# Performance work log

Measured on AMD Instinct MI355X. Metric: run time of the kernel, lower is better.

Reference implementation:

```python
import jax, jax.numpy as jnp
import numpy as np

# dims
B, L, H, W, C = 1, 5, 100, 176, 256   # batch, agents, BEV height, BEV width, channels
HEADS, DHEAD, T = 8, 32, 3            # heads, per-head dim, num agent types
D = HEADS * DHEAD                     # == C here (to_qkv inner dim)
SCALE = DHEAD ** -0.5


def setup_inputs() -> dict:
    key = jax.random.key(0)
    ks = jax.random.split(key, 14)
    x = jax.random.normal(ks[0], (B, L, H, W, C), jnp.float32)
    mask = jnp.ones((B, H, W, 1, L), jnp.int32)
    types = jax.random.randint(ks[1], (B, L), 0, T)
    # prior_encoding: [B, L, 1, 1, 3] = (velocity, dt, type); only type (channel 2) is used
    prior_encoding = jnp.zeros((B, L, 1, 1, 3), jnp.float32).at[..., 2].set(
        types[:, :, None, None].astype(jnp.float32))
    s = C ** -0.5
    Wq = jax.random.normal(ks[2], (T, C, D), jnp.float32) * s
    bq = jax.random.normal(ks[3], (T, D), jnp.float32) * 0.01
    Wk = jax.random.normal(ks[4], (T, C, D), jnp.float32) * s
    bk = jax.random.normal(ks[5], (T, D), jnp.float32) * 0.01
    Wv = jax.random.normal(ks[6], (T, C, D), jnp.float32) * s
    bv = jax.random.normal(ks[7], (T, D), jnp.float32) * 0.01
    Wa = jax.random.normal(ks[8], (T, D, C), jnp.float32) * (D ** -0.5)
    ba = jax.random.normal(ks[9], (T, C), jnp.float32) * 0.01
    rel_att = jax.random.normal(ks[10], (T * T, HEADS, DHEAD, DHEAD), jnp.float32) * (DHEAD ** -0.5)
    rel_msg = jax.random.normal(ks[11], (T * T, HEADS, DHEAD, DHEAD), jnp.float32) * (DHEAD ** -0.5)
    return dict(x=x, mask=mask, prior_encoding=prior_encoding,
                Wq=Wq, bq=bq, Wk=Wk, bk=bk, Wv=Wv, bv=bv, Wa=Wa, ba=ba,
                rel_att=rel_att, rel_msg=rel_msg)


def _split_heads(t):
    # [B,H,W,L,D] -> [B,m,H,W,L,p]
    return jnp.transpose(t.reshape(B, H, W, L, HEADS, DHEAD), (0, 4, 1, 2, 3, 5))


def reference(x, mask, prior_encoding, Wq, bq, Wk, bk, Wv, bv, Wa, ba, rel_att, rel_msg):
    types = prior_encoding[:, :, 0, 0, 2].astype(jnp.int32)      # [B,L]
    xp = jnp.transpose(x, (0, 2, 3, 1, 4))                        # [B,H,W,L,C]

    def proj(Wt, bt):
        # per-agent-type linear: gather weights per agent, then batched matmul
        return jnp.einsum('bhwlc,blcd->bhwld', xp, Wt[types]) + bt[types][:, None, None]

    q = _split_heads(proj(Wq, bq))                                # [B,m,H,W,L,p]
    k = _split_heads(proj(Wk, bk))
    v = _split_heads(proj(Wv, bv))

    etype = types[:, :, None] * T + types[:, None, :]             # [B,L,L]
    w_att = jnp.transpose(rel_att[etype], (0, 3, 1, 2, 4, 5))     # [B,m,L,L,p,q]
    w_msg = jnp.transpose(rel_msg[etype], (0, 3, 1, 2, 4, 5))     # [B,m,L,L,p,c]

    att = jnp.einsum('bmhwip,bmijpq,bmhwjq->bmhwij', q, w_att, k) * SCALE
    att = jnp.where(mask[:, None] == 0, -jnp.inf, att)            # mask [B,1,H,W,1,L]
    att = jax.nn.softmax(att, axis=-1)

    v_msg = jnp.einsum('bmijpc,bmhwjp->bmhwijc', w_msg, v)        # relation-weighted messages
    out = jnp.einsum('bmhwij,bmhwijc->bmhwic', att, v_msg)        # [B,m,H,W,L,c]

    out = jnp.transpose(out, (0, 2, 3, 4, 1, 5)).reshape(B, H, W, L, D)
    out = jnp.einsum('bhwld,bldc->bhwlc', out, Wa[types]) + ba[types][:, None, None]
    return jnp.transpose(out, (0, 3, 1, 2, 4))                    # [B,L,H,W,C]
```

## Files before the change

### kernel.cpp

```cpp
#include <hip/hip_runtime.h>
#include <math.h>

#define HW     17600
#define CD     256
#define LAG    5
#define NHEAD  8
#define DH     32
#define NT     3

typedef short bf16x8 __attribute__((ext_vector_type(8)));
typedef float f32x4  __attribute__((ext_vector_type(4)));

__device__ __forceinline__ float bflo(unsigned u) { return __uint_as_float(u << 16); }
__device__ __forceinline__ float bfhi(unsigned u) { return __uint_as_float(u & 0xffff0000u); }
__device__ __forceinline__ unsigned f2bf(float f) {
    unsigned u = __float_as_uint(f);
    return (u + 0x7fffu + ((u >> 16) & 1u)) >> 16;
}
__device__ __forceinline__ unsigned pack2(float a, float b) {
    return f2bf(a) | (f2bf(b) << 16);
}

__global__ __launch_bounds__(256) void convert_w_kernel(
    const float* __restrict__ Wq, const float* __restrict__ Wk,
    const float* __restrict__ Wv, const float* __restrict__ Wa,
    unsigned short* __restrict__ Wt)
{
    __shared__ float tile[64][65];
    const int mat = blockIdx.y;
    const int k0 = (blockIdx.x >> 2) * 64;
    const int n0 = (blockIdx.x & 3) * 64;
    const float* W;
    if      (mat < 3) W = Wq + (long)mat * 65536;
    else if (mat < 6) W = Wk + (long)(mat - 3) * 65536;
    else if (mat < 9) W = Wv + (long)(mat - 6) * 65536;
    else              W = Wa + (long)(mat - 9) * 65536;
    const int t = threadIdx.x;
#pragma unroll
    for (int r = 0; r < 16; ++r) {
        int idx = r * 256 + t;
        int row = idx >> 6, col = idx & 63;
        tile[row][col] = W[(long)(k0 + row) * 256 + n0 + col];
    }
    __syncthreads();
    unsigned short* dst = Wt + (long)mat * 65536;
#pragma unroll
    for (int r = 0; r < 16; ++r) {
        int idx = r * 256 + t;
        int row = idx >> 6, col = idx & 63;
        dst[(long)(n0 + row) * 256 + k0 + col] = (unsigned short)f2bf(tile[col][row]);
    }
}

__global__ __launch_bounds__(256) void convert_rel_kernel(
    const float* __restrict__ rel_att, const float* __restrict__ rel_msg,
    unsigned short* __restrict__ rattT, unsigned short* __restrict__ rmsgT)
{
    const long base = ((long)(blockIdx.x * NHEAD + blockIdx.y)) << 10;
    const int t = threadIdx.x;
#pragma unroll
    for (int i = 0; i < 4; ++i) {
        int idx = t * 4 + i;
        int p = idx >> 5, q = idx & 31;
        rattT[base + q * 32 + p] = (unsigned short)f2bf(rel_att[base + idx]);
        rmsgT[base + q * 32 + p] = (unsigned short)f2bf(rel_msg[base + idx]);
    }
}

template<bool AF32, bool YBF>
__device__ __forceinline__ void gemm_mfma_core(
    const void* __restrict__ Aptr, long lda,
    const unsigned short* __restrict__ Wt,
    const float* __restrict__ bias,
    void* __restrict__ Yptr, long ldy)
{
    __shared__ unsigned short As[64 * 64];
    __shared__ unsigned short Ws[256 * 64];

    const int t  = threadIdx.x;
    const int m0 = blockIdx.x * 64;
    const int w  = t >> 6;
    const int l  = t & 63;
    const int wr = w >> 1;
    const int wc = w & 1;
    const int fr = l & 15;
    const int ko = (l >> 4) << 3;

    const int srow = t >> 3;
    const int colu = (t & 7) << 3;
    const int scol = colu ^ ((srow & 7) << 3);
    const int axor = (fr & 7) << 3;

    f32x4 acc[2][8];
#pragma unroll
    for (int i = 0; i < 2; ++i)
#pragma unroll
        for (int j = 0; j < 8; ++j) {
            acc[i][j][0] = 0.f; acc[i][j][1] = 0.f;
            acc[i][j][2] = 0.f; acc[i][j][3] = 0.f;
        }

    for (int ks = 0; ks < 4; ++ks) {
        const int k0 = ks << 6;
        __syncthreads();
#pragma unroll
        for (int r = 0; r < 2; ++r) {
            int row = r * 32 + srow;
            if (AF32) {
                const float* src = (const float*)Aptr + (long)(m0 + row) * lda + k0 + colu;
                float4 f0 = *(const float4*)src;
                float4 f1 = *(const float4*)(src + 4);
                uint4 u;
                u.x = pack2(f0.x, f0.y); u.y = pack2(f0.z, f0.w);
                u.z = pack2(f1.x, f1.y); u.w = pack2(f1.z, f1.w);
                *(uint4*)(&As[row * 64 + scol]) = u;
            } else {
                const unsigned short* src =
                    (const unsigned short*)Aptr + (long)(m0 + row) * lda + k0 + colu;
                *(uint4*)(&As[row * 64 + scol]) = *(const uint4*)src;
            }
        }
#pragma unroll
        for (int r = 0; r < 8; ++r) {
            int row = r * 32 + srow;
            *(uint4*)(&Ws[row * 64 + scol]) =
                *(const uint4*)(Wt + (long)row * 256 + k0 + colu);
        }
        __syncthreads();
#pragma unroll
        for (int kk = 0; kk < 2; ++kk) {
            const int fcol = ((kk << 5) | ko) ^ axor;
            bf16x8 a[2], b[8];
#pragma unroll
            for (int i = 0; i < 2; ++i)
                a[i] = *(const bf16x8*)(&As[(wr * 32 + i * 16 + fr) * 64 + fcol]);
#pragma unroll
            for (int j = 0; j < 8; ++j)
                b[j] = *(const bf16x8*)(&Ws[(wc * 128 + j * 16 + fr) * 64 + fcol]);
#pragma unroll
            for (int i = 0; i < 2; ++i)
#pragma unroll
                for (int j = 0; j < 8; ++j)
                    acc[i][j] = __builtin_amdgcn_mfma_f32_16x16x32_bf16(
                        a[i], b[j], acc[i][j], 0, 0, 0);
        }
    }

    const int fq = l >> 4;
#pragma unroll
    for (int j = 0; j < 8; ++j) {
        int col = wc * 128 + j * 16 + fr;
        float bz = bias[col];
#pragma unroll
        for (int i = 0; i < 2; ++i) {
            int rowb = m0 + wr * 32 + i * 16 + (fq << 2);
#pragma unroll
            for (int e = 0; e < 4; ++e) {
                float v = acc[i][j][e] + bz;
                if (YBF)
                    ((unsigned short*)Yptr)[(long)(rowb + e) * ldy + col] =
                        (unsigned short)f2bf(v);
                else
                    ((float*)Yptr)[(long)(rowb + e) * ldy + col] = v;
            }
        }
    }
}

__global__ __launch_bounds__(256) void gemm_qkv_mfma(
    const float* __restrict__ x, const float* __restrict__ pe,
    const unsigned short* __restrict__ Wt,
    const float* __restrict__ bq, const float* __restrict__ bk,
    const float* __restrict__ bv,
    unsigned short* __restrict__ qws, unsigned short* __restrict__ kws,
    unsigned short* __restrict__ vws)
{
    const int z = blockIdx.z;
    const int lag = z / 3, proj = z % 3;
    const int tpe = (int)pe[lag * 3 + 2];
    const float* A = x + (long)lag * HW * CD;
    const unsigned short* Wm = Wt + (long)(proj * 3 + tpe) * 65536;
    const float* bias;
    unsigned short* Y;
    long ldy;
    if      (proj == 0) { bias = bq; Y = qws + (long)lag * CD; ldy = LAG * CD; }
    else if (proj == 1) { bias = bk; Y = kws + (long)lag * HW * CD; ldy = CD; }
    else                { bias = bv; Y = vws + (long)lag * HW * CD; ldy = CD; }
    bias += tpe * CD;
    gemm_mfma_core<true, true>(A, CD, Wm, bias, Y, ldy);
}

__global__ __launch_bounds__(256) void gemm_out_mfma(
    const unsigned short* __restrict__ aws, const float* __restrict__ pe,
    const unsigned short* __restrict__ Wt, const float* __restrict__ ba,
    float* __restrict__ out)
{
    const int lag = blockIdx.z;
    const int tpe = (int)pe[lag * 3 + 2];
    const unsigned short* A = aws + (long)lag * CD;
    const unsigned short* Wm = Wt + (long)(9 + tpe) * 65536;
    const float* bias = ba + tpe * CD;
    float* Y = out + (long)lag * HW * CD;
    gemm_mfma_core<false, false>(A, (long)LAG * CD, Wm, bias, Y, CD);
}

#define QTROW 488
#define VGROW 168

__global__ __launch_bounds__(256) void attn_fused_kernel(
    const unsigned short* __restrict__ qws,
    const unsigned short* __restrict__ kws,
    const unsigned short* __restrict__ vws,
    const unsigned short* __restrict__ rattT,
    const unsigned short* __restrict__ rmsgT,
    const int* __restrict__ mask, const float* __restrict__ pe,
    unsigned short* __restrict__ aws)
{
    __shared__ unsigned short lds[4 * 16 * QTROW];

    const int t    = threadIdx.x;
    const int w    = t >> 6;
    const int l    = t & 63;
    const int fr   = l & 15;
    const int fq   = l >> 4;
    const int m    = blockIdx.y;
    const int pix0 = blockIdx.x * 64;

    const int pl2   = t >> 2;
    const int sub   = t & 3;
    const int gpix2 = pix0 + pl2;

    int ty[LAG];
#pragma unroll
    for (int i = 0; i < LAG; ++i) ty[i] = (int)pe[i * 3 + 2];
    bool pres[NT] = {false, false, false};
#pragma unroll
    for (int i = 0; i < LAG; ++i) {
        pres[0] = pres[0] || (ty[i] == 0);
        pres[1] = pres[1] || (ty[i] == 1);
        pres[2] = pres[2] || (ty[i] == 2);
    }

    uint4 kf[LAG], vf[LAG];
    int mk[LAG];
#pragma unroll
    for (int j = 0; j < LAG; ++j) {
        const long off = ((long)j * HW + gpix2) * CD + m * DH + sub * 8;
        kf[j] = *(const uint4*)(kws + off);
        vf[j] = *(const uint4*)(vws + off);
        mk[j] = mask[gpix2 * LAG + j];
    }

    {
        bf16x8 aq[LAG];
#pragma unroll
        for (int i = 0; i < LAG; ++i)
            aq[i] = *(const bf16x8*)(qws + (long)(pix0 + w * 16 + fr) * (LAG * CD)
                                     + i * CD + m * DH + fq * 8);
        const int qtbase = w * 16 * QTROW;
#pragma unroll
        for (int sg = 0; sg < NT; ++sg) {
            if (!pres[sg]) continue;
#pragma unroll
            for (int i = 0; i < LAG; ++i) {
                const int e = ty[i] * NT + sg;
                const unsigned short* bb = rattT + ((long)(e * NHEAD + m) << 10);
                bf16x8 b0 = *(const bf16x8*)(bb + fr * 32 + fq * 8);
                bf16x8 b1 = *(const bf16x8*)(bb + (fr + 16) * 32 + fq * 8);
                f32x4 z = {0.f, 0.f, 0.f, 0.f};
                f32x4 d0 = __builtin_amdgcn_mfma_f32_16x16x32_bf16(aq[i], b0, z, 0, 0, 0);
                f32x4 d1 = __builtin_amdgcn_mfma_f32_16x16x32_bf16(aq[i], b1, z, 0, 0, 0);
#pragma unroll
                for (int e4 = 0; e4 < 4; ++e4) {
                    const int idx = qtbase + (fq * 4 + e4) * QTROW + (i * NT + sg) * 32;
                    lds[idx + fr]      = (unsigned short)f2bf(d0[e4]);
                    lds[idx + fr + 16] = (unsigned short)f2bf(d1[e4]);
                }
            }
        }
    }
    __syncthreads();

    const float scale = 0.17677669529663687f;
    float att[LAG][LAG];
    {
        const int qtb = w * 16 * QTROW + (pl2 & 15) * QTROW;
#pragma unroll
        for (int j = 0; j < LAG; ++j) {
            float kx[8];
            kx[0] = bflo(kf[j].x); kx[1] = bfhi(kf[j].x);
            kx[2] = bflo(kf[j].y); kx[3] = bfhi(kf[j].y);
            kx[4] = bflo(kf[j].z); kx[5] = bfhi(kf[j].z);
            kx[6] = bflo(kf[j].w); kx[7] = bfhi(kf[j].w);
            const int tyj = ty[j];
#pragma unroll
            for (int i = 0; i < LAG; ++i) {
                uint4 qv = *(const uint4*)(&lds[qtb + (i * NT + tyj) * 32 + sub * 8]);
                float part;
                part = bflo(qv.x) * kx[0];
                part = fmaf(bfhi(qv.x), kx[1], part);
                part = fmaf(bflo(qv.y), kx[2], part);
                part = fmaf(bfhi(qv.y), kx[3], part);
                part = fmaf(bflo(qv.z), kx[4], part);
                part = fmaf(bfhi(qv.z), kx[5], part);
                part = fmaf(bflo(qv.w), kx[6], part);
                part = fmaf(bfhi(qv.w), kx[7], part);
                part += __shfl_xor(part, 1);
                part += __shfl_xor(part, 2);
                att[i][j] = part * scale;
            }
        }
#pragma unroll
        for (int i = 0; i < LAG; ++i) {
            float mx = -INFINITY;
#pragma unroll
            for (int j = 0; j < LAG; ++j) {
                att[i][j] = mk[j] ? att[i][j] : -INFINITY;
                mx = fmaxf(mx, att[i][j]);
            }
            float ssum = 0.f;
#pragma unroll
            for (int j = 0; j < LAG; ++j) {
                att[i][j] = __expf(att[i][j] - mx);
                ssum += att[i][j];
            }
            float inv = 1.f / ssum;
#pragma unroll
            for (int j = 0; j < LAG; ++j) att[i][j] *= inv;
        }
    }

    float vx[LAG][8];
#pragma unroll
    for (int j = 0; j < LAG; ++j) {
        vx[j][0] = bflo(vf[j].x); vx[j][1] = bfhi(vf[j].x);
        vx[j][2] = bflo(vf[j].y); vx[j][3] = bfhi(vf[j].y);
        vx[j][4] = bflo(vf[j].z); vx[j][5] = bfhi(vf[j].z);
        vx[j][6] = bflo(vf[j].w); vx[j][7] = bfhi(vf[j].w);
    }

    f32x4 oacc[LAG][2];
#pragma unroll
    for (int i = 0; i < LAG; ++i)
#pragma unroll
        for (int c = 0; c < 2; ++c) {
            oacc[i][c][0] = 0.f; oacc[i][c][1] = 0.f;
            oacc[i][c][2] = 0.f; oacc[i][c][3] = 0.f;
        }

    const int vgw = w * 16 * QTROW;
    for (int sg = 0; sg < NT; ++sg) {
        if (!pres[sg]) continue;
        __syncthreads();
#pragma unroll
        for (int i = 0; i < LAG; ++i) {
            float vg[8] = {0.f,0.f,0.f,0.f,0.f,0.f,0.f,0.f};
#pragma unroll
            for (int j = 0; j < LAG; ++j) {
                float wj = (ty[j] == sg) ? att[i][j] : 0.f;
#pragma unroll
                for (int d = 0; d < 8; ++d) vg[d] = fmaf(wj, vx[j][d], vg[d]);
            }
            uint4 o;
            o.x = pack2(vg[0], vg[1]); o.y = pack2(vg[2], vg[3]);
            o.z = pack2(vg[4], vg[5]); o.w = pack2(vg[6], vg[7]);
            *(uint4*)(&lds[vgw + (pl2 & 15) * VGROW + i * 32 + sub * 8]) = o;
        }
        __syncthreads();
#pragma unroll
        for (int i = 0; i < LAG; ++i) {
            bf16x8 a = *(const bf16x8*)(&lds[vgw + fr * VGROW + i * 32 + fq * 8]);
            const int e = ty[i] * NT + sg;
            const unsigned short* bb = rmsgT + ((long)(e * NHEAD + m) << 10);
            bf16x8 b0 = *(const bf16x8*)(bb + fr * 32 + fq * 8);
            bf16x8 b1 = *(const bf16x8*)(bb + (fr + 16) * 32 + fq * 8);
            oacc[i][0] = __builtin_amdgcn_mfma_f32_16x16x32_bf16(a, b0, oacc[i][0], 0, 0, 0);
            oacc[i][1] = __builtin_amdgcn_mfma_f32_16x16x32_bf16(a, b1, oacc[i][1], 0, 0, 0);
        }
    }

#pragma unroll
    for (int i = 0; i < LAG; ++i) {
#pragma unroll
        for (int e4 = 0; e4 < 4; ++e4) {
            const long ob = (long)(pix0 + w * 16 + fq * 4 + e4) * (LAG * CD)
                            + i * CD + m * DH;
            aws[ob + fr]      = (unsigned short)f2bf(oacc[i][0][e4]);
            aws[ob + fr + 16] = (unsigned short)f2bf(oacc[i][1][e4]);
        }
    }
}

extern "C" void kernel_launch(void* const* d_in, const int* in_sizes, int n_in,
                              void* d_out, int out_size, void* d_ws, size_t ws_size,
                              hipStream_t stream) {
    const float* x    = (const float*)d_in[0];
    const int*   mask = (const int*)  d_in[1];
    const float* pe   = (const float*)d_in[2];
    const float* Wq   = (const float*)d_in[3];
    const float* bq   = (const float*)d_in[4];
    const float* Wk   = (const float*)d_in[5];
    const float* bk   = (const float*)d_in[6];
    const float* Wv   = (const float*)d_in[7];
    const float* bv   = (const float*)d_in[8];
    const float* Wa   = (const float*)d_in[9];
    const float* ba   = (const float*)d_in[10];
    const float* ratt = (const float*)d_in[11];
    const float* rmsg = (const float*)d_in[12];
    float* out = (float*)d_out;

    const size_t PLANE = (size_t)LAG * HW * CD;

    unsigned short* qws   = (unsigned short*)d_ws;
    unsigned short* kws   = qws + PLANE;
    unsigned short* vws   = kws + PLANE;
    unsigned short* aws   = vws + PLANE;
    unsigned short* Wt    = aws + PLANE;
    unsigned short* rattT = Wt + 786432;
    unsigned short* rmsgT = rattT + 73728;

    convert_w_kernel<<<dim3(16, 12), 256, 0, stream>>>(Wq, Wk, Wv, Wa, Wt);
    convert_rel_kernel<<<dim3(9, 8), 256, 0, stream>>>(ratt, rmsg, rattT, rmsgT);

    gemm_qkv_mfma<<<dim3(HW / 64, 1, LAG * 3), 256, 0, stream>>>(
        x, pe, Wt, bq, bk, bv, qws, kws, vws);

    attn_fused_kernel<<<dim3(HW / 64, NHEAD), 256, 0, stream>>>(
        qws, kws, vws, rattT, rmsgT, mask, pe, aws);

    gemm_out_mfma<<<dim3(HW / 64, 1, LAG), 256, 0, stream>>>(aws, pe, Wt, ba, out);
}
```

Baseline: 210.2 us.

## Pre-convert x to bf16 and shrink attention LDS by per-type staging

```diff
diff --git a/kernel.cpp b/kernel.cpp
--- a/kernel.cpp
+++ b/kernel.cpp
@@ -19,6 +19,18 @@
 }
 __device__ __forceinline__ unsigned pack2(float a, float b) {
     return f2bf(a) | (f2bf(b) << 16);
+}
+
+__global__ __launch_bounds__(256) void convert_x_kernel(
+    const float* __restrict__ x, unsigned short* __restrict__ xb)
+{
+    const long i = ((long)blockIdx.x * 256 + threadIdx.x) * 8;
+    float4 f0 = *(const float4*)(x + i);
+    float4 f1 = *(const float4*)(x + i + 4);
+    uint4 u;
+    u.x = pack2(f0.x, f0.y); u.y = pack2(f0.z, f0.w);
+    u.z = pack2(f1.x, f1.y); u.w = pack2(f1.z, f1.w);
+    *(uint4*)(xb + i) = u;
 }
 
 __global__ __launch_bounds__(256) void convert_w_kernel(
@@ -67,9 +79,9 @@
     }
 }
 
-template<bool AF32, bool YBF>
+template<bool YBF>
 __device__ __forceinline__ void gemm_mfma_core(
-    const void* __restrict__ Aptr, long lda,
+    const unsigned short* __restrict__ Aptr, long lda,
     const unsigned short* __restrict__ Wt,
     const float* __restrict__ bias,
     void* __restrict__ Yptr, long ldy)
@@ -106,19 +118,8 @@
 #pragma unroll
         for (int r = 0; r < 2; ++r) {
             int row = r * 32 + srow;
-            if (AF32) {
-                const float* src = (const float*)Aptr + (long)(m0 + row) * lda + k0 + colu;
-                float4 f0 = *(const float4*)src;
-                float4 f1 = *(const float4*)(src + 4);
-                uint4 u;
-                u.x = pack2(f0.x, f0.y); u.y = pack2(f0.z, f0.w);
-                u.z = pack2(f1.x, f1.y); u.w = pack2(f1.z, f1.w);
-                *(uint4*)(&As[row * 64 + scol]) = u;
-            } else {
-                const unsigned short* src =
-                    (const unsigned short*)Aptr + (long)(m0 + row) * lda + k0 + colu;
-                *(uint4*)(&As[row * 64 + scol]) = *(const uint4*)src;
-            }
+            const unsigned short* src = Aptr + (long)(m0 + row) * lda + k0 + colu;
+            *(uint4*)(&As[row * 64 + scol]) = *(const uint4*)src;
         }
 #pragma unroll
         for (int r = 0; r < 8; ++r) {
@@ -168,7 +169,7 @@
 }
 
 __global__ __launch_bounds__(256) void gemm_qkv_mfma(
-    const float* __restrict__ x, const float* __restrict__ pe,
+    const unsigned short* __restrict__ xb, const float* __restrict__ pe,
     const unsigned short* __restrict__ Wt,
     const float* __restrict__ bq, const float* __restrict__ bk,
     const float* __restrict__ bv,
@@ -178,7 +179,7 @@
     const int z = blockIdx.z;
     const int lag = z / 3, proj = z % 3;
     const int tpe = (int)pe[lag * 3 + 2];
-    const float* A = x + (long)lag * HW * CD;
+    const unsigned short* A = xb + (long)lag * HW * CD;
     const unsigned short* Wm = Wt + (long)(proj * 3 + tpe) * 65536;
     const float* bias;
     unsigned short* Y;
@@ -187,7 +188,7 @@
     else if (proj == 1) { bias = bk; Y = kws + (long)lag * HW * CD; ldy = CD; }
     else                { bias = bv; Y = vws + (long)lag * HW * CD; ldy = CD; }
     bias += tpe * CD;
-    gemm_mfma_core<true, true>(A, CD, Wm, bias, Y, ldy);
+    gemm_mfma_core<true>(A, CD, Wm, bias, Y, ldy);
 }
 
 __global__ __launch_bounds__(256) void gemm_out_mfma(
@@ -201,10 +202,9 @@
     const unsigned short* Wm = Wt + (long)(9 + tpe) * 65536;
     const float* bias = ba + tpe * CD;
     float* Y = out + (long)lag * HW * CD;
-    gemm_mfma_core<false, false>(A, (long)LAG * CD, Wm, bias, Y, CD);
-}
-
-#define QTROW 488
+    gemm_mfma_core<false>(A, (long)LAG * CD, Wm, bias, Y, CD);
+}
+
 #define VGROW 168
 
 __global__ __launch_bounds__(256) void attn_fused_kernel(
@@ -216,7 +216,7 @@
     const int* __restrict__ mask, const float* __restrict__ pe,
     unsigned short* __restrict__ aws)
 {
-    __shared__ unsigned short lds[4 * 16 * QTROW];
+    __shared__ unsigned short lds[4 * 16 * VGROW];
 
     const int t    = threadIdx.x;
     const int w    = t >> 6;
@@ -229,6 +229,8 @@
     const int pl2   = t >> 2;
     const int sub   = t & 3;
     const int gpix2 = pix0 + pl2;
+    const int wbase = w * 16 * VGROW;
+    const int qtb   = wbase + (pl2 & 15) * VGROW;
 
     int ty[LAG];
 #pragma unroll
@@ -241,102 +243,99 @@
         pres[2] = pres[2] || (ty[i] == 2);
     }
 
-    uint4 kf[LAG], vf[LAG];
+    uint4 kf[LAG];
     int mk[LAG];
 #pragma unroll
     for (int j = 0; j < LAG; ++j) {
-        const long off = ((long)j * HW + gpix2) * CD + m * DH + sub * 8;
-        kf[j] = *(const uint4*)(kws + off);
-        vf[j] = *(const uint4*)(vws + off);
+        kf[j] = *(const uint4*)(kws + ((long)j * HW + gpix2) * CD + m * DH + sub * 8);
         mk[j] = mask[gpix2 * LAG + j];
     }
-
-    {
-        bf16x8 aq[LAG];
-#pragma unroll
-        for (int i = 0; i < LAG; ++i)
-            aq[i] = *(const bf16x8*)(qws + (long)(pix0 + w * 16 + fr) * (LAG * CD)
-                                     + i * CD + m * DH + fq * 8);
-        const int qtbase = w * 16 * QTROW;
-#pragma unroll
-        for (int sg = 0; sg < NT; ++sg) {
-            if (!pres[sg]) continue;
-#pragma unroll
-            for (int i = 0; i < LAG; ++i) {
-                const int e = ty[i] * NT + sg;
-                const unsigned short* bb = rattT + ((long)(e * NHEAD + m) << 10);
-                bf16x8 b0 = *(const bf16x8*)(bb + fr * 32 + fq * 8);
-                bf16x8 b1 = *(const bf16x8*)(bb + (fr + 16) * 32 + fq * 8);
-                f32x4 z = {0.f, 0.f, 0.f, 0.f};
-                f32x4 d0 = __builtin_amdgcn_mfma_f32_16x16x32_bf16(aq[i], b0, z, 0, 0, 0);
-                f32x4 d1 = __builtin_amdgcn_mfma_f32_16x16x32_bf16(aq[i], b1, z, 0, 0, 0);
-#pragma unroll
-                for (int e4 = 0; e4 < 4; ++e4) {
-                    const int idx = qtbase + (fq * 4 + e4) * QTROW + (i * NT + sg) * 32;
-                    lds[idx + fr]      = (unsigned short)f2bf(d0[e4]);
-                    lds[idx + fr + 16] = (unsigned short)f2bf(d1[e4]);
-                }
-            }
-        }
-    }
-    __syncthreads();
+    bf16x8 aq[LAG];
+#pragma unroll
+    for (int i = 0; i < LAG; ++i)
+        aq[i] = *(const bf16x8*)(qws + (long)(pix0 + w * 16 + fr) * (LAG * CD)
+                                 + i * CD + m * DH + fq * 8);
+
+    float kx[LAG][8];
+#pragma unroll
+    for (int j = 0; j < LAG; ++j) {
+        kx[j][0] = bflo(kf[j].x); kx[j][1] = bfhi(kf[j].x);
+        kx[j][2] = bflo(kf[j].y); kx[j][3] = bfhi(kf[j].y);
+        kx[j][4] = bflo(kf[j].z); kx[j][5] = bfhi(kf[j].z);
+        kx[j][6] = bflo(kf[j].w); kx[j][7] = bfhi(kf[j].w);
+    }
 
     const float scale = 0.17677669529663687f;
     float att[LAG][LAG];
-    {
-        const int qtb = w * 16 * QTROW + (pl2 & 15) * QTROW;
+    for (int sg = 0; sg < NT; ++sg) {
+        if (!pres[sg]) continue;
+#pragma unroll
+        for (int i = 0; i < LAG; ++i) {
+            const int e = ty[i] * NT + sg;
+            const unsigned short* bb = rattT + ((long)(e * NHEAD + m) << 10);
+            bf16x8 b0 = *(const bf16x8*)(bb + fr * 32 + fq * 8);
+            bf16x8 b1 = *(const bf16x8*)(bb + (fr + 16) * 32 + fq * 8);
+            f32x4 z = {0.f, 0.f, 0.f, 0.f};
+            f32x4 d0 = __builtin_amdgcn_mfma_f32_16x16x32_bf16(aq[i], b0, z, 0, 0, 0);
+            f32x4 d1 = __builtin_amdgcn_mfma_f32_16x16x32_bf16(aq[i], b1, z, 0, 0, 0);
+#pragma unroll
+            for (int e4 = 0; e4 < 4; ++e4) {
+                const int idx = wbase + (fq * 4 + e4) * VGROW + i * 32;
+                lds[idx + fr]      = (unsigned short)f2bf(d0[e4]);
+                lds[idx + fr + 16] = (unsigned short)f2bf(d1[e4]);
+            }
+        }
+        __syncthreads();
 #pragma unroll
         for (int j = 0; j < LAG; ++j) {
-            float kx[8];
-            kx[0] = bflo(kf[j].x); kx[1] = bfhi(kf[j].x);
-            kx[2] = bflo(kf[j].y); kx[3] = bfhi(kf[j].y);
-            kx[4] = bflo(kf[j].z); kx[5] = bfhi(kf[j].z);
-            kx[6] = bflo(kf[j].w); kx[7] = bfhi(kf[j].w);
-            const int tyj = ty[j];
+            if (ty[j] != sg) continue;
 #pragma unroll
             for (int i = 0; i < LAG; ++i) {
-                uint4 qv = *(const uint4*)(&lds[qtb + (i * NT + tyj) * 32 + sub * 8]);
+                uint4 qv = *(const uint4*)(&lds[qtb + i * 32 + sub * 8]);
                 float part;
-                part = bflo(qv.x) * kx[0];
-                part = fmaf(bfhi(qv.x), kx[1], part);
-                part = fmaf(bflo(qv.y), kx[2], part);
-                part = fmaf(bfhi(qv.y), kx[3], part);
-                part = fmaf(bflo(qv.z), kx[4], part);
-                part = fmaf(bfhi(qv.z), kx[5], part);
-                part = fmaf(bflo(qv.w), kx[6], part);
-                part = fmaf(bfhi(qv.w), kx[7], part);
+                part = bflo(qv.x) * kx[j][0];
+                part = fmaf(bfhi(qv.x), kx[j][1], part);
+                part = fmaf(bflo(qv.y), kx[j][2], part);
+                part = fmaf(bfhi(qv.y), kx[j][3], part);
+                part = fmaf(bflo(qv.z), kx[j][4], part);
+                part = fmaf(bfhi(qv.z), kx[j][5], part);
+                part = fmaf(bflo(qv.w), kx[j][6], part);
+                part = fmaf(bfhi(qv.w), kx[j][7], part);
                 part += __shfl_xor(part, 1);
                 part += __shfl_xor(part, 2);
                 att[i][j] = part * scale;
             }
         }
-#pragma unroll
-        for (int i = 0; i < LAG; ++i) {
-            float mx = -INFINITY;
-#pragma unroll
-            for (int j = 0; j < LAG; ++j) {
-                att[i][j] = mk[j] ? att[i][j] : -INFINITY;
-                mx = fmaxf(mx, att[i][j]);
-            }
-            float ssum = 0.f;
-#pragma unroll
-            for (int j = 0; j < LAG; ++j) {
-                att[i][j] = __expf(att[i][j] - mx);
-                ssum += att[i][j];
-            }
-            float inv = 1.f / ssum;
-#pragma unroll
-            for (int j = 0; j < LAG; ++j) att[i][j] *= inv;
-        }
+        __syncthreads();
+    }
+
+#pragma unroll
+    for (int i = 0; i < LAG; ++i) {
+        float mx = -INFINITY;
+#pragma unroll
+        for (int j = 0; j < LAG; ++j) {
+            att[i][j] = mk[j] ? att[i][j] : -INFINITY;
+            mx = fmaxf(mx, att[i][j]);
+        }
+        float ssum = 0.f;
+#pragma unroll
+        for (int j = 0; j < LAG; ++j) {
+            att[i][j] = __expf(att[i][j] - mx);
+            ssum += att[i][j];
+        }
+        float inv = 1.f / ssum;
+#pragma unroll
+        for (int j = 0; j < LAG; ++j) att[i][j] *= inv;
     }
 
     float vx[LAG][8];
 #pragma unroll
     for (int j = 0; j < LAG; ++j) {
-        vx[j][0] = bflo(vf[j].x); vx[j][1] = bfhi(vf[j].x);
-        vx[j][2] = bflo(vf[j].y); vx[j][3] = bfhi(vf[j].y);
-        vx[j][4] = bflo(vf[j].z); vx[j][5] = bfhi(vf[j].z);
-        vx[j][6] = bflo(vf[j].w); vx[j][7] = bfhi(vf[j].w);
+        uint4 vf = *(const uint4*)(vws + ((long)j * HW + gpix2) * CD + m * DH + sub * 8);
+        vx[j][0] = bflo(vf.x); vx[j][1] = bfhi(vf.x);
+        vx[j][2] = bflo(vf.y); vx[j][3] = bfhi(vf.y);
+        vx[j][4] = bflo(vf.z); vx[j][5] = bfhi(vf.z);
+        vx[j][6] = bflo(vf.w); vx[j][7] = bfhi(vf.w);
     }
 
     f32x4 oacc[LAG][2];
@@ -348,10 +347,8 @@
             oacc[i][c][2] = 0.f; oacc[i][c][3] = 0.f;
         }
 
-    const int vgw = w * 16 * QTROW;
     for (int sg = 0; sg < NT; ++sg) {
         if (!pres[sg]) continue;
-        __syncthreads();
 #pragma unroll
         for (int i = 0; i < LAG; ++i) {
             float vg[8] = {0.f,0.f,0.f,0.f,0.f,0.f,0.f,0.f};
@@ -364,12 +361,12 @@
             uint4 o;
             o.x = pack2(vg[0], vg[1]); o.y = pack2(vg[2], vg[3]);
             o.z = pack2(vg[4], vg[5]); o.w = pack2(vg[6], vg[7]);
-            *(uint4*)(&lds[vgw + (pl2 & 15) * VGROW + i * 32 + sub * 8]) = o;
+            *(uint4*)(&lds[qtb + i * 32 + sub * 8]) = o;
         }
         __syncthreads();
 #pragma unroll
         for (int i = 0; i < LAG; ++i) {
-            bf16x8 a = *(const bf16x8*)(&lds[vgw + fr * VGROW + i * 32 + fq * 8]);
+            bf16x8 a = *(const bf16x8*)(&lds[wbase + fr * VGROW + i * 32 + fq * 8]);
             const int e = ty[i] * NT + sg;
             const unsigned short* bb = rmsgT + ((long)(e * NHEAD + m) << 10);
             bf16x8 b0 = *(const bf16x8*)(bb + fr * 32 + fq * 8);
@@ -377,6 +374,7 @@
             oacc[i][0] = __builtin_amdgcn_mfma_f32_16x16x32_bf16(a, b0, oacc[i][0], 0, 0, 0);
             oacc[i][1] = __builtin_amdgcn_mfma_f32_16x16x32_bf16(a, b1, oacc[i][1], 0, 0, 0);
         }
+        __syncthreads();
     }
 
 #pragma unroll
@@ -415,15 +413,17 @@
     unsigned short* kws   = qws + PLANE;
     unsigned short* vws   = kws + PLANE;
     unsigned short* aws   = vws + PLANE;
-    unsigned short* Wt    = aws + PLANE;
+    unsigned short* xb    = aws + PLANE;
+    unsigned short* Wt    = xb + PLANE;
     unsigned short* rattT = Wt + 786432;
     unsigned short* rmsgT = rattT + 73728;
 
     convert_w_kernel<<<dim3(16, 12), 256, 0, stream>>>(Wq, Wk, Wv, Wa, Wt);
     convert_rel_kernel<<<dim3(9, 8), 256, 0, stream>>>(ratt, rmsg, rattT, rmsgT);
+    convert_x_kernel<<<dim3(11000), 256, 0, stream>>>(x, xb);
 
     gemm_qkv_mfma<<<dim3(HW / 64, 1, LAG * 3), 256, 0, stream>>>(
-        x, pe, Wt, bq, bk, bv, qws, kws, vws);
+        xb, pe, Wt, bq, bk, bv, qws, kws, vws);
 
     attn_fused_kernel<<<dim3(HW / 64, NHEAD), 256, 0, stream>>>(
         qws, kws, vws, rattT, rmsgT, mask, pe, aws);
```

Result: slower. 296.2 us (+40.9%).

## Use 128-row GEMM tiles with 512 threads and fuse QKV projections per block

Applied to the files above, without the earlier changes.

```diff
diff --git a/kernel.cpp b/kernel.cpp
--- a/kernel.cpp
+++ b/kernel.cpp
@@ -68,17 +68,17 @@
 }
 
 template<bool AF32, bool YBF>
-__device__ __forceinline__ void gemm_mfma_core(
+__device__ __forceinline__ void gemm_mfma_core128(
     const void* __restrict__ Aptr, long lda,
     const unsigned short* __restrict__ Wt,
     const float* __restrict__ bias,
-    void* __restrict__ Yptr, long ldy)
-{
-    __shared__ unsigned short As[64 * 64];
+    void* __restrict__ Yptr, long ldy, int mlim)
+{
+    __shared__ unsigned short As[128 * 64];
     __shared__ unsigned short Ws[256 * 64];
 
     const int t  = threadIdx.x;
-    const int m0 = blockIdx.x * 64;
+    const int m0 = blockIdx.x * 128;
     const int w  = t >> 6;
     const int l  = t & 63;
     const int wr = w >> 1;
@@ -88,7 +88,6 @@
 
     const int srow = t >> 3;
     const int colu = (t & 7) << 3;
-    const int scol = colu ^ ((srow & 7) << 3);
     const int axor = (fr & 7) << 3;
 
     f32x4 acc[2][8];
@@ -105,9 +104,11 @@
         __syncthreads();
 #pragma unroll
         for (int r = 0; r < 2; ++r) {
-            int row = r * 32 + srow;
+            int row = r * 64 + srow;
+            int grow = m0 + row; if (grow >= mlim) grow = mlim - 1;
+            int scol = colu ^ ((row & 7) << 3);
             if (AF32) {
-                const float* src = (const float*)Aptr + (long)(m0 + row) * lda + k0 + colu;
+                const float* src = (const float*)Aptr + (long)grow * lda + k0 + colu;
                 float4 f0 = *(const float4*)src;
                 float4 f1 = *(const float4*)(src + 4);
                 uint4 u;
@@ -116,13 +117,14 @@
                 *(uint4*)(&As[row * 64 + scol]) = u;
             } else {
                 const unsigned short* src =
-                    (const unsigned short*)Aptr + (long)(m0 + row) * lda + k0 + colu;
+                    (const unsigned short*)Aptr + (long)grow * lda + k0 + colu;
                 *(uint4*)(&As[row * 64 + scol]) = *(const uint4*)src;
             }
         }
 #pragma unroll
-        for (int r = 0; r < 8; ++r) {
-            int row = r * 32 + srow;
+        for (int r = 0; r < 4; ++r) {
+            int row = r * 64 + srow;
+            int scol = colu ^ ((row & 7) << 3);
             *(uint4*)(&Ws[row * 64 + scol]) =
                 *(const uint4*)(Wt + (long)row * 256 + k0 + colu);
         }
@@ -156,18 +158,20 @@
             int rowb = m0 + wr * 32 + i * 16 + (fq << 2);
 #pragma unroll
             for (int e = 0; e < 4; ++e) {
+                int row = rowb + e;
+                if (row >= mlim) continue;
                 float v = acc[i][j][e] + bz;
                 if (YBF)
-                    ((unsigned short*)Yptr)[(long)(rowb + e) * ldy + col] =
+                    ((unsigned short*)Yptr)[(long)row * ldy + col] =
                         (unsigned short)f2bf(v);
                 else
-                    ((float*)Yptr)[(long)(rowb + e) * ldy + col] = v;
-            }
-        }
-    }
-}
-
-__global__ __launch_bounds__(256) void gemm_qkv_mfma(
+                    ((float*)Yptr)[(long)row * ldy + col] = v;
+            }
+        }
+    }
+}
+
+__global__ __launch_bounds__(512) void gemm_qkv_mfma(
     const float* __restrict__ x, const float* __restrict__ pe,
     const unsigned short* __restrict__ Wt,
     const float* __restrict__ bq, const float* __restrict__ bk,
@@ -175,22 +179,26 @@
     unsigned short* __restrict__ qws, unsigned short* __restrict__ kws,
     unsigned short* __restrict__ vws)
 {
-    const int z = blockIdx.z;
-    const int lag = z / 3, proj = z % 3;
+    const int lag = blockIdx.z;
     const int tpe = (int)pe[lag * 3 + 2];
     const float* A = x + (long)lag * HW * CD;
-    const unsigned short* Wm = Wt + (long)(proj * 3 + tpe) * 65536;
-    const float* bias;
-    unsigned short* Y;
-    long ldy;
-    if      (proj == 0) { bias = bq; Y = qws + (long)lag * CD; ldy = LAG * CD; }
-    else if (proj == 1) { bias = bk; Y = kws + (long)lag * HW * CD; ldy = CD; }
-    else                { bias = bv; Y = vws + (long)lag * HW * CD; ldy = CD; }
-    bias += tpe * CD;
-    gemm_mfma_core<true, true>(A, CD, Wm, bias, Y, ldy);
-}
-
-__global__ __launch_bounds__(256) void gemm_out_mfma(
+
+#pragma unroll 1
+    for (int proj = 0; proj < 3; ++proj) {
+        const unsigned short* Wm = Wt + (long)(proj * 3 + tpe) * 65536;
+        const float* bias;
+        unsigned short* Y;
+        long ldy;
+        if      (proj == 0) { bias = bq; Y = qws + (long)lag * CD; ldy = LAG * CD; }
+        else if (proj == 1) { bias = bk; Y = kws + (long)lag * HW * CD; ldy = CD; }
+        else                { bias = bv; Y = vws + (long)lag * HW * CD; ldy = CD; }
+        bias += tpe * CD;
+        gemm_mfma_core128<true, true>(A, CD, Wm, bias, Y, ldy, HW);
+        __syncthreads();
+    }
+}
+
+__global__ __launch_bounds__(512) void gemm_out_mfma(
     const unsigned short* __restrict__ aws, const float* __restrict__ pe,
     const unsigned short* __restrict__ Wt, const float* __restrict__ ba,
     float* __restrict__ out)
@@ -201,7 +209,7 @@
     const unsigned short* Wm = Wt + (long)(9 + tpe) * 65536;
     const float* bias = ba + tpe * CD;
     float* Y = out + (long)lag * HW * CD;
-    gemm_mfma_core<false, false>(A, (long)LAG * CD, Wm, bias, Y, CD);
+    gemm_mfma_core128<false, false>(A, (long)LAG * CD, Wm, bias, Y, CD, HW);
 }
 
 #define QTROW 488
@@ -422,11 +430,12 @@
     convert_w_kernel<<<dim3(16, 12), 256, 0, stream>>>(Wq, Wk, Wv, Wa, Wt);
     convert_rel_kernel<<<dim3(9, 8), 256, 0, stream>>>(ratt, rmsg, rattT, rmsgT);
 
-    gemm_qkv_mfma<<<dim3(HW / 64, 1, LAG * 3), 256, 0, stream>>>(
+    gemm_qkv_mfma<<<dim3((HW + 127) / 128, 1, LAG), 512, 0, stream>>>(
         x, pe, Wt, bq, bk, bv, qws, kws, vws);
 
     attn_fused_kernel<<<dim3(HW / 64, NHEAD), 256, 0, stream>>>(
         qws, kws, vws, rattT, rmsgT, mask, pe, aws);
 
-    gemm_out_mfma<<<dim3(HW / 64, 1, LAG), 256, 0, stream>>>(aws, pe, Wt, ba, out);
-}
+    gemm_out_mfma<<<dim3((HW + 127) / 128, 1, LAG), 512, 0, stream>>>(
+        aws, pe, Wt, ba, out);
+}
```

Measured after the change: 275.8 us. 31.2% more time.
